# Optimization experiments

Measured on AMD Instinct MI355X. Metric: run time of the kernel, lower is better.

## Reference

```python
import jax, jax.numpy as jnp
import numpy as np

N0, N1, N2 = 120000, 40000, 10000   # sampled node counts per hop
E0, E1 = 600000, 150000             # edges per block (fanout ~15)
DIN, DH, NC = 128, 256, 47


def _glorot(k, fan_in, fan_out):
    s = (2.0 / (fan_in + fan_out)) ** 0.5
    return jax.random.normal(k, (fan_in, fan_out), jnp.float32) * s


def setup_inputs() -> dict:
    key = jax.random.key(0)
    ks = jax.random.split(key, 20)
    x0 = jax.random.normal(ks[0], (N0, DIN), jnp.float32)
    src0 = jax.random.randint(ks[1], (E0,), 0, N0)
    dst0 = jax.random.randint(ks[2], (E0,), 0, N1)
    src1 = jax.random.randint(ks[3], (E1,), 0, N1)
    dst1 = jax.random.randint(ks[4], (E1,), 0, N2)
    srcb0 = jax.random.randint(ks[5], (E0,), 0, N0)
    dstb0 = jax.random.randint(ks[6], (E0,), 0, N1)
    srcb1 = jax.random.randint(ks[7], (E1,), 0, N1)
    dstb1 = jax.random.randint(ks[8], (E1,), 0, N2)
    # id_old_value_new: must satisfy idx[:n] < n for every truncation length n,
    # i.e. idx[k] in [0, k+1)
    rng = np.random.default_rng(0)
    idx = jnp.asarray((rng.random(N0) * (np.arange(N0) + 1)).astype(np.int64))
    mix_ratio = jnp.float32(0.5)
    Wl0 = _glorot(ks[9], DIN, DH); Wr0 = _glorot(ks[10], DIN, DH)
    b0 = jnp.zeros((DH,), jnp.float32)
    Wl1 = _glorot(ks[11], DH, DH); Wr1 = _glorot(ks[12], DH, DH)
    b1 = jnp.zeros((DH,), jnp.float32)
    Wlin = _glorot(ks[13], DH, NC)
    blin = jnp.zeros((NC,), jnp.float32)
    return dict(x0=x0, src0=src0, dst0=dst0, src1=src1, dst1=dst1,
                srcb0=srcb0, dstb0=dstb0, srcb1=srcb1, dstb1=dstb1,
                idx=idx, mix_ratio=mix_ratio,
                Wl0=Wl0, Wr0=Wr0, b0=b0, Wl1=Wl1, Wr1=Wr1, b1=b1,
                Wlin=Wlin, blin=blin)


def _sage(x_all, root_x, src, dst, n_root, Wl, Wr, b):
    # PyG-style SAGEConv, mean aggregation: lin_l(mean_j x_j) + lin_r(root)
    msgs = x_all[src]                                        # [E, D] gather
    s = jax.ops.segment_sum(msgs, dst, num_segments=n_root)  # [n_root, D]
    cnt = jax.ops.segment_sum(jnp.ones_like(dst, dtype=x_all.dtype), dst,
                              num_segments=n_root)
    mean = s / jnp.maximum(cnt, 1.0)[:, None]
    return mean @ Wl + root_x @ Wr + b


def reference(x0, src0, dst0, src1, dst1, srcb0, dstb0, srcb1, dstb1,
              idx, mix_ratio, Wl0, Wr0, b0, Wl1, Wr1, b1, Wlin, blin):
    blocks = [(src0, dst0, N1), (src1, dst1, N2)]
    blocks_b = [(srcb0, dstb0, N1), (srcb1, dstb1, N2)]
    params = [(Wl0, Wr0, b0), (Wl1, Wr1, b1)]
    m = mix_ratio

    # first branch (dropout omitted: inference mode)
    aggr_xs = [x0]
    for i in range(2):
        src, dst, n_root = blocks[i]
        Wl, Wr, b = params[i]
        root_x = aggr_xs[-1][:n_root]
        x = jax.nn.relu(_sage(aggr_xs[-1], root_x, src, dst, n_root, Wl, Wr, b))
        aggr_xs.append(x)

    # permuted branch via id_old_value_new gather
    aggr_xs_b = [x[idx[: x.shape[0]]] for x in aggr_xs]

    x_mix = aggr_xs[0] * m + aggr_xs_b[0] * (1.0 - m)
    for i in range(2):
        src, dst, n_root = blocks[i]
        srcb, dstb, n_root_b = blocks_b[i]
        Wl, Wr, b = params[i]
        x_new = jax.nn.relu(_sage(aggr_xs[i], x_mix[:n_root], src, dst,
                                  n_root, Wl, Wr, b))
        x_new_b = jax.nn.relu(_sage(aggr_xs_b[i], x_mix[:n_root_b], srcb, dstb,
                                    n_root_b, Wl, Wr, b))
        x_mix = x_new * m + x_new_b * (1.0 - m)

    logits = x_mix @ Wlin + blin
    return jax.nn.log_softmax(logits, axis=-1)
```

## Files before the change

### kernel.cpp

```cpp
#include <hip/hip_runtime.h>
#include <math.h>

#define N1C 40000
#define N2C 10000
#define DIN 128
#define DH  256
#define NC  47

#define TOTCNT (2 * N1C + 2 * N2C)
#define CAP 64
#define CURSTR 16

typedef __attribute__((ext_vector_type(8))) short v8s;
typedef __attribute__((ext_vector_type(4))) float v4f;
typedef __attribute__((ext_vector_type(2))) float v2f;

#if __has_builtin(__builtin_amdgcn_cvt_pk_f32_fp8)
#define HW_FP8 1
#endif

__device__ __forceinline__ unsigned short f2bf(float f) {
    unsigned int u = __float_as_uint(f);
    u += 0x7FFF + ((u >> 16) & 1);
    return (unsigned short)(u >> 16);
}
__device__ __forceinline__ float bf2f(unsigned int h) {
    return __uint_as_float(h << 16);
}

__device__ __forceinline__ unsigned char f2e4m3(float f) {
    unsigned int u = __float_as_uint(f);
    unsigned char s = (unsigned char)((u >> 24) & 0x80);
    float a = __uint_as_float(u & 0x7FFFFFFF);
    if (a > 448.0f) a = 448.0f;
    if (a < 0.015625f) {
        int k = (int)rintf(a * 512.0f);
        return s | (unsigned char)k;
    }
    unsigned int bits = __float_as_uint(a);
    int et = (int)(bits >> 23) - 127 + 7;
    unsigned int m32 = bits & 0x7FFFFF;
    unsigned int m3 = m32 >> 20;
    unsigned int rest = m32 & 0xFFFFF;
    if (rest > 0x80000 || (rest == 0x80000 && (m3 & 1))) m3++;
    if (m3 == 8) { m3 = 0; et++; }
    if (et > 15 || (et == 15 && m3 == 7)) return s | 0x7E;
    return s | (unsigned char)((et << 3) | m3);
}

__device__ __forceinline__ void dec4(unsigned int u, float& f0, float& f1,
                                     float& f2, float& f3) {
#ifdef HW_FP8
    v2f lo = __builtin_amdgcn_cvt_pk_f32_fp8((int)u, false);
    v2f hi = __builtin_amdgcn_cvt_pk_f32_fp8((int)u, true);
    f0 = lo[0]; f1 = lo[1]; f2 = hi[0]; f3 = hi[1];
#else
    auto d1 = [](unsigned int b) -> float {
        int e = (b >> 3) & 15, mm = b & 7;
        float d = (e == 0) ? (float)mm * (1.0f / 512.0f)
                           : (1.0f + (float)mm * 0.125f) * exp2f((float)(e - 7));
        return (b & 0x80) ? -d : d;
    };
    f0 = d1(u & 0xFF); f1 = d1((u >> 8) & 0xFF);
    f2 = d1((u >> 16) & 0xFF); f3 = d1(u >> 24);
#endif
}

__global__ __launch_bounds__(256) void front_fused(
        const int* __restrict__ src0, const int* __restrict__ dst0,
        const int* __restrict__ srcb0, const int* __restrict__ dstb0,
        const int* __restrict__ src1, const int* __restrict__ dst1,
        const int* __restrict__ srcb1, const int* __restrict__ dstb1,
        const int* __restrict__ perm, int* __restrict__ cur,
        int* __restrict__ bucket, int E0, int E1, int nbFill,
        const float* __restrict__ x0, unsigned char* __restrict__ x0f,
        long n8, int nbConv,
        const float* __restrict__ Wl0, const float* __restrict__ Wr0,
        const float* __restrict__ Wl1, const float* __restrict__ Wr1,
        unsigned short* __restrict__ Wt0l, unsigned short* __restrict__ Wt0r,
        unsigned short* __restrict__ Wt1l, unsigned short* __restrict__ Wt1r) {
    int b = blockIdx.x, t = threadIdx.x;
    if (b < nbFill) {
        int e = b * 256 + t;
        int tot = 2 * E0 + 2 * E1;
        if (e >= tot) return;
        int s, bin;
        if (e < E0) {
            s = src0[e];                  bin = dst0[e];
        } else if (e < 2 * E0) {
            int le = e - E0;
            s = perm[srcb0[le]];          bin = N1C + dstb0[le];
        } else if (e < 2 * E0 + E1) {
            int le = e - 2 * E0;
            s = src1[le];                 bin = 2 * N1C + dst1[le];
        } else {
            int le = e - 2 * E0 - E1;
            s = perm[srcb1[le]];          bin = 2 * N1C + N2C + dstb1[le];
        }
        int pos = atomicAdd(&cur[(size_t)bin * CURSTR], 1);
        if (pos < CAP) bucket[(size_t)bin * CAP + pos] = s;
    } else if (b < nbFill + nbConv) {
        long i = (long)(b - nbFill) * 256 + t;
        if (i >= n8) return;
        const float4* p = (const float4*)(x0 + i * 8);
        float4 a = p[0], c = p[1];
        float f[8] = {a.x, a.y, a.z, a.w, c.x, c.y, c.z, c.w};
        unsigned int q0 = 0, q1 = 0;
#pragma unroll
        for (int j = 0; j < 8; j++) {
            unsigned int e8 = f2e4m3(f[j]);
            if (j < 4) q0 |= e8 << (8 * j); else q1 |= e8 << (8 * (j - 4));
        }
        uint2 q = {q0, q1};
        *(uint2*)(x0f + i * 8) = q;
    } else {
        int id = (b - nbFill - nbConv) * 256 + t;
        const int S0 = DIN * DH;
        const int S1 = DH * DH;
        const float* W; unsigned short* Wt; int K, loc;
        if (id < S0)                   { W = Wl0; Wt = Wt0l; K = DIN; loc = id; }
        else if (id < 2 * S0)          { W = Wr0; Wt = Wt0r; K = DIN; loc = id - S0; }
        else if (id < 2 * S0 + S1)     { W = Wl1; Wt = Wt1l; K = DH;  loc = id - 2 * S0; }
        else if (id < 2 * S0 + 2 * S1) { W = Wr1; Wt = Wt1r; K = DH;  loc = id - 2 * S0 - S1; }
        else return;
        int n = loc / K, k = loc - n * K;
        Wt[(size_t)n * K + k] = f2bf(W[(size_t)k * DH + n]);
    }
}

__global__ __launch_bounds__(256) void gather_mean_128f(
        const unsigned char* __restrict__ xf, const int* __restrict__ bucket,
        const int* __restrict__ cur, unsigned short* __restrict__ mean0,
        unsigned short* __restrict__ meanb0) {
    const int half = N1C / 8;
    int b = blockIdx.x;
    int binbase; unsigned short* outp; int rb;
    if (b < half) { binbase = 0;   outp = mean0;  rb = b; }
    else          { binbase = N1C; outp = meanb0; rb = b - half; }
    int wv = threadIdx.x >> 6, lane = threadIdx.x & 63;
    int row = rb * 8 + wv * 2 + (lane >> 5);
    int c4 = (lane & 31) * 4;
    int bin = binbase + row;
    int cnt = min(cur[(size_t)bin * CURSTR], CAP);
    const int* cs = bucket + (size_t)bin * CAP;
    float a0 = 0.0f, a1 = 0.0f, a2 = 0.0f, a3 = 0.0f;
    int i = 0;
    for (; i + 3 < cnt; i += 4) {
        int s0 = cs[i], s1 = cs[i + 1], s2 = cs[i + 2], s3 = cs[i + 3];
        unsigned int u = *(const unsigned int*)&xf[(size_t)s0 * DIN + c4];
        unsigned int v = *(const unsigned int*)&xf[(size_t)s1 * DIN + c4];
        unsigned int w = *(const unsigned int*)&xf[(size_t)s2 * DIN + c4];
        unsigned int z = *(const unsigned int*)&xf[(size_t)s3 * DIN + c4];
        float u0, u1, u2, u3, w0, w1, w2, w3, p0, p1, p2, p3, q0, q1, q2, q3;
        dec4(u, u0, u1, u2, u3);
        dec4(v, w0, w1, w2, w3);
        dec4(w, p0, p1, p2, p3);
        dec4(z, q0, q1, q2, q3);
        a0 += (u0 + w0) + (p0 + q0); a1 += (u1 + w1) + (p1 + q1);
        a2 += (u2 + w2) + (p2 + q2); a3 += (u3 + w3) + (p3 + q3);
    }
    for (; i < cnt; i++) {
        unsigned int u = *(const unsigned int*)&xf[(size_t)cs[i] * DIN + c4];
        float u0, u1, u2, u3;
        dec4(u, u0, u1, u2, u3);
        a0 += u0; a1 += u1; a2 += u2; a3 += u3;
    }
    float inv = 1.0f / (float)max(cnt, 1);
    uint2 o;
    o.x = (unsigned int)f2bf(a0 * inv) | ((unsigned int)f2bf(a1 * inv) << 16);
    o.y = (unsigned int)f2bf(a2 * inv) | ((unsigned int)f2bf(a3 * inv) << 16);
    *(uint2*)&outp[(size_t)row * DIN + c4] = o;
}

__global__ __launch_bounds__(256) void gather_mean_256f(
        const unsigned char* __restrict__ xf, const int* __restrict__ bucket,
        const int* __restrict__ cur, unsigned short* __restrict__ mean1,
        unsigned short* __restrict__ meanb1) {
    const int half = N2C / 4;
    int b = blockIdx.x;
    int binbase; unsigned short* outp; int rb;
    if (b < half) { binbase = 2 * N1C;       outp = mean1;  rb = b; }
    else          { binbase = 2 * N1C + N2C; outp = meanb1; rb = b - half; }
    int row = rb * 4 + (threadIdx.x >> 6);
    int lane = threadIdx.x & 63;
    int bin = binbase + row;
    int cnt = min(cur[(size_t)bin * CURSTR], CAP);
    const int* cs = bucket + (size_t)bin * CAP;
    float a0 = 0.0f, a1 = 0.0f, a2 = 0.0f, a3 = 0.0f;
    int i = 0;
    for (; i + 3 < cnt; i += 4) {
        int s0 = cs[i], s1 = cs[i + 1], s2 = cs[i + 2], s3 = cs[i + 3];
        unsigned int u = *(const unsigned int*)&xf[(size_t)s0 * DH + lane * 4];
        unsigned int v = *(const unsigned int*)&xf[(size_t)s1 * DH + lane * 4];
        unsigned int w = *(const unsigned int*)&xf[(size_t)s2 * DH + lane * 4];
        unsigned int z = *(const unsigned int*)&xf[(size_t)s3 * DH + lane * 4];
        float u0, u1, u2, u3, w0, w1, w2, w3, p0, p1, p2, p3, q0, q1, q2, q3;
        dec4(u, u0, u1, u2, u3);
        dec4(v, w0, w1, w2, w3);
        dec4(w, p0, p1, p2, p3);
        dec4(z, q0, q1, q2, q3);
        a0 += (u0 + w0) + (p0 + q0); a1 += (u1 + w1) + (p1 + q1);
        a2 += (u2 + w2) + (p2 + q2); a3 += (u3 + w3) + (p3 + q3);
    }
    for (; i < cnt; i++) {
        unsigned int u = *(const unsigned int*)&xf[(size_t)cs[i] * DH + lane * 4];
        float u0, u1, u2, u3;
        dec4(u, u0, u1, u2, u3);
        a0 += u0; a1 += u1; a2 += u2; a3 += u3;
    }
    float inv = 1.0f / (float)max(cnt, 1);
    uint2 o;
    o.x = (unsigned int)f2bf(a0 * inv) | ((unsigned int)f2bf(a1 * inv) << 16);
    o.y = (unsigned int)f2bf(a2 * inv) | ((unsigned int)f2bf(a3 * inv) << 16);
    *(uint2*)&outp[(size_t)row * DH + lane * 4] = o;
}

#define KP0 136
#define H0T 5
__global__ __launch_bounds__(256, 2) void hop0_mfma(
        const float* __restrict__ x0, const int* __restrict__ idx,
        const unsigned short* __restrict__ mean0, const unsigned short* __restrict__ meanb0,
        const unsigned short* __restrict__ Wtl, const unsigned short* __restrict__ Wtr,
        const float* __restrict__ b, const float* __restrict__ mixp,
        unsigned char* __restrict__ x1f, unsigned short* __restrict__ xm1) {
    __shared__ unsigned short Alds[4][16][KP0];
    int t = threadIdx.x;
    int wv = t >> 6, lane = t & 63;
    int mrow = lane & 15, quad = lane >> 4;
    float m = *mixp;

    v8s wl[4][4], wr[4][4];
    float bb[4];
#pragma unroll
    for (int ct = 0; ct < 4; ct++) {
        int n = wv * 64 + mrow * 4 + ct;
        bb[ct] = b[n];
#pragma unroll
        for (int ks = 0; ks < 4; ks++) {
            int k0 = ks * 32 + quad * 8;
            wl[ct][ks] = *(const v8s*)&Wtl[(size_t)n * DIN + k0];
            wr[ct][ks] = *(const v8s*)&Wtr[(size_t)n * DIN + k0];
        }
    }

    for (int tile = 0; tile < H0T; tile++) {
        int row0 = (blockIdx.x * H0T + tile) * 16;
        {
            int r = t >> 4, k0 = (t & 15) * 8;
            int rg = row0 + r;
            *(v8s*)&Alds[0][r][k0] = *(const v8s*)&mean0[(size_t)rg * DIN + k0];
            *(v8s*)&Alds[1][r][k0] = *(const v8s*)&meanb0[(size_t)rg * DIN + k0];
            const float4* xr4 = (const float4*)&x0[(size_t)rg * DIN + k0];
            float4 A0 = xr4[0], A1 = xr4[1];
            int ib = idx[rg];
            const float4* xb4 = (const float4*)&x0[(size_t)ib * DIN + k0];
            float4 B0 = xb4[0], B1 = xb4[1];
            float fa[8] = {A0.x, A0.y, A0.z, A0.w, A1.x, A1.y, A1.z, A1.w};
            float fb[8] = {B0.x, B0.y, B0.z, B0.w, B1.x, B1.y, B1.z, B1.w};
            v8s vr, vm;
#pragma unroll
            for (int j = 0; j < 8; j++) {
                vr[j] = (short)f2bf(fa[j]);
                vm[j] = (short)f2bf(m * fa[j] + (1.0f - m) * fb[j]);
            }
            *(v8s*)&Alds[2][r][k0] = vr;
            *(v8s*)&Alds[3][r][k0] = vm;
        }
        __syncthreads();
        v4f accA[4], accB[4], accC[4], accD[4];
#pragma unroll
        for (int ct = 0; ct < 4; ct++) {
            accA[ct] = (v4f){0.f, 0.f, 0.f, 0.f}; accB[ct] = (v4f){0.f, 0.f, 0.f, 0.f};
            accC[ct] = (v4f){0.f, 0.f, 0.f, 0.f}; accD[ct] = (v4f){0.f, 0.f, 0.f, 0.f};
        }
#pragma unroll
        for (int ks = 0; ks < 4; ks++) {
            int k0 = ks * 32 + quad * 8;
            v8s aM = *(v8s*)&Alds[0][mrow][k0];
            v8s aB = *(v8s*)&Alds[1][mrow][k0];
            v8s aR = *(v8s*)&Alds[2][mrow][k0];
            v8s aX = *(v8s*)&Alds[3][mrow][k0];
#pragma unroll
            for (int ct = 0; ct < 4; ct++) {
                accA[ct] = __builtin_amdgcn_mfma_f32_16x16x32_bf16(aM, wl[ct][ks], accA[ct], 0, 0, 0);
                accB[ct] = __builtin_amdgcn_mfma_f32_16x16x32_bf16(aB, wl[ct][ks], accB[ct], 0, 0, 0);
                accC[ct] = __builtin_amdgcn_mfma_f32_16x16x32_bf16(aR, wr[ct][ks], accC[ct], 0, 0, 0);
                accD[ct] = __builtin_amdgcn_mfma_f32_16x16x32_bf16(aX, wr[ct][ks], accD[ct], 0, 0, 0);
            }
        }
        int colb = wv * 64 + mrow * 4;
#pragma unroll
        for (int r = 0; r < 4; r++) {
            int row = row0 + quad * 4 + r;
            unsigned int xpack = 0;
            unsigned int s01, s23;
            unsigned short sh[4];
#pragma unroll
            for (int ct = 0; ct < 4; ct++) {
                float pA = accA[ct][r], pB = accB[ct][r], pC = accC[ct][r], pD = accD[ct][r];
                float xv  = fmaxf(pA + pC + bb[ct], 0.0f);
                float xn  = fmaxf(pA + pD + bb[ct], 0.0f);
                float xnb = fmaxf(pB + pD + bb[ct], 0.0f);
                xpack |= ((unsigned int)f2e4m3(xv)) << (8 * ct);
                sh[ct] = f2bf(m * xn + (1.0f - m) * xnb);
            }
            s01 = (unsigned int)sh[0] | ((unsigned int)sh[1] << 16);
            s23 = (unsigned int)sh[2] | ((unsigned int)sh[3] << 16);
            *(unsigned int*)&x1f[(size_t)row * DH + colb] = xpack;
            uint2 xm = {s01, s23};
            *(uint2*)&xm1[(size_t)row * DH + colb] = xm;
        }
        __syncthreads();
    }
}

#define KP1 264
#define H1T 2
__global__ __launch_bounds__(256, 2) void hop1_mfma(
        const unsigned short* __restrict__ mean1, const unsigned short* __restrict__ meanb1,
        const unsigned short* __restrict__ xm1,
        const unsigned short* __restrict__ Wtl, const unsigned short* __restrict__ Wtr,
        const float* __restrict__ b, const float* __restrict__ mixp,
        float* __restrict__ xm2) {
    __shared__ unsigned short Alds[3][16][KP1];
    int t = threadIdx.x;
    int wv = t >> 6, lane = t & 63;
    int mrow = lane & 15, quad = lane >> 4;
    float m = *mixp;

    v8s wlc[4][4], wrc[4][4];
    float bb[4];
#pragma unroll
    for (int ct = 0; ct < 4; ct++) {
        int n = wv * 64 + mrow * 4 + ct;
        bb[ct] = b[n];
#pragma unroll
        for (int ks = 0; ks < 4; ks++) {
            int k0 = ks * 32 + quad * 8;
            wlc[ct][ks] = *(const v8s*)&Wtl[(size_t)n * DH + k0];
            wrc[ct][ks] = *(const v8s*)&Wtr[(size_t)n * DH + k0];
        }
    }

    for (int tt = 0; tt < H1T; tt++) {
        int tIdx = blockIdx.x * H1T + tt;
        if (tIdx >= N2C / 16) break;
        int row0 = tIdx * 16;
        {
            int r = t >> 4, k0 = (t & 15) * 16;
            int rg = row0 + r;
            *(v8s*)&Alds[0][r][k0]     = *(const v8s*)&mean1[(size_t)rg * DH + k0];
            *(v8s*)&Alds[0][r][k0 + 8] = *(const v8s*)&mean1[(size_t)rg * DH + k0 + 8];
            *(v8s*)&Alds[1][r][k0]     = *(const v8s*)&meanb1[(size_t)rg * DH + k0];
            *(v8s*)&Alds[1][r][k0 + 8] = *(const v8s*)&meanb1[(size_t)rg * DH + k0 + 8];
            *(v8s*)&Alds[2][r][k0]     = *(const v8s*)&xm1[(size_t)rg * DH + k0];
            *(v8s*)&Alds[2][r][k0 + 8] = *(const v8s*)&xm1[(size_t)rg * DH + k0 + 8];
        }
        __syncthreads();
        v4f accA[4], accB[4], accC[4];
#pragma unroll
        for (int ct = 0; ct < 4; ct++) {
            accA[ct] = (v4f){0.f, 0.f, 0.f, 0.f};
            accB[ct] = (v4f){0.f, 0.f, 0.f, 0.f};
            accC[ct] = (v4f){0.f, 0.f, 0.f, 0.f};
        }
#pragma unroll
        for (int ks = 0; ks < 8; ks++) {
            int k0 = ks * 32 + quad * 8;
            v8s aM = *(v8s*)&Alds[0][mrow][k0];
            v8s aB = *(v8s*)&Alds[1][mrow][k0];
            v8s aR = *(v8s*)&Alds[2][mrow][k0];
#pragma unroll
            for (int ct = 0; ct < 4; ct++) {
                v8s bl, br;
                if (ks < 4) { bl = wlc[ct][ks]; br = wrc[ct][ks]; }
                else {
                    int n = wv * 64 + mrow * 4 + ct;
                    bl = *(const v8s*)&Wtl[(size_t)n * DH + k0];
                    br = *(const v8s*)&Wtr[(size_t)n * DH + k0];
                }
                accA[ct] = __builtin_amdgcn_mfma_f32_16x16x32_bf16(aM, bl, accA[ct], 0, 0, 0);
                accB[ct] = __builtin_amdgcn_mfma_f32_16x16x32_bf16(aB, bl, accB[ct], 0, 0, 0);
                accC[ct] = __builtin_amdgcn_mfma_f32_16x16x32_bf16(aR, br, accC[ct], 0, 0, 0);
            }
        }
        int colb = wv * 64 + mrow * 4;
#pragma unroll
        for (int r = 0; r < 4; r++) {
            int row = row0 + quad * 4 + r;
            float4 o;
            float v0 = fmaxf(accA[0][r] + accC[0][r] + bb[0], 0.0f);
            float w0 = fmaxf(accB[0][r] + accC[0][r] + bb[0], 0.0f);
            float v1 = fmaxf(accA[1][r] + accC[1][r] + bb[1], 0.0f);
            float w1 = fmaxf(accB[1][r] + accC[1][r] + bb[1], 0.0f);
            float v2 = fmaxf(accA[2][r] + accC[2][r] + bb[2], 0.0f);
            float w2 = fmaxf(accB[2][r] + accC[2][r] + bb[2], 0.0f);
            float v3 = fmaxf(accA[3][r] + accC[3][r] + bb[3], 0.0f);
            float w3 = fmaxf(accB[3][r] + accC[3][r] + bb[3], 0.0f);
            o.x = m * v0 + (1.0f - m) * w0;
            o.y = m * v1 + (1.0f - m) * w1;
            o.z = m * v2 + (1.0f - m) * w2;
            o.w = m * v3 + (1.0f - m) * w3;
            *(float4*)&xm2[(size_t)row * DH + colb] = o;
        }
        __syncthreads();
    }
}

__global__ __launch_bounds__(256) void logits_lsm(
        const float* __restrict__ xmix2, const float* __restrict__ Wlin,
        const float* __restrict__ blin, float* __restrict__ out, int nrows) {
    int w = threadIdx.x >> 6;
    int row = blockIdx.x * 4 + w;
    int t = threadIdx.x & 63;
    __shared__ float xs[4][DH];
    if (row < nrows)
        for (int i = t; i < DH; i += 64) xs[w][i] = xmix2[(size_t)row * DH + i];
    __syncthreads();
    if (row >= nrows) return;
    float acc = 0.0f;
    if (t < NC) {
        acc = blin[t];
        for (int k = 0; k < DH; k++) acc += xs[w][k] * Wlin[k * NC + t];
    }
    float v = (t < NC) ? acc : -INFINITY;
    float mx = v;
    for (int off = 32; off; off >>= 1) mx = fmaxf(mx, __shfl_xor(mx, off, 64));
    float ex = (t < NC) ? expf(acc - mx) : 0.0f;
    float sum = ex;
    for (int off = 32; off; off >>= 1) sum += __shfl_xor(sum, off, 64);
    if (t < NC) out[(size_t)row * NC + t] = acc - mx - logf(sum);
}

extern "C" void kernel_launch(void* const* d_in, const int* in_sizes, int n_in,
                              void* d_out, int out_size, void* d_ws, size_t ws_size,
                              hipStream_t stream) {
    const float* x0    = (const float*)d_in[0];
    const int*   src0  = (const int*)d_in[1];
    const int*   dst0  = (const int*)d_in[2];
    const int*   src1  = (const int*)d_in[3];
    const int*   dst1  = (const int*)d_in[4];
    const int*   srcb0 = (const int*)d_in[5];
    const int*   dstb0 = (const int*)d_in[6];
    const int*   srcb1 = (const int*)d_in[7];
    const int*   dstb1 = (const int*)d_in[8];
    const int*   idx   = (const int*)d_in[9];
    const float* mixp  = (const float*)d_in[10];
    const float* Wl0   = (const float*)d_in[11];
    const float* Wr0   = (const float*)d_in[12];
    const float* b0    = (const float*)d_in[13];
    const float* Wl1   = (const float*)d_in[14];
    const float* Wr1   = (const float*)d_in[15];
    const float* b1    = (const float*)d_in[16];
    const float* Wlin  = (const float*)d_in[17];
    const float* blin  = (const float*)d_in[18];
    float* out = (float*)d_out;

    const int E0 = in_sizes[1];
    const int E1 = in_sizes[3];
    const long x0elems = (long)in_sizes[0];

    int* wsi    = (int*)d_ws;
    int* cur    = wsi;
    int* bucket = cur + (size_t)TOTCNT * CURSTR;
    unsigned short* wsh = (unsigned short*)(bucket + (size_t)TOTCNT * CAP);
    unsigned short* mean0  = wsh;
    unsigned short* meanb0 = mean0  + (size_t)N1C * DIN;
    unsigned short* mean1  = meanb0 + (size_t)N1C * DIN;
    unsigned short* meanb1 = mean1  + (size_t)N2C * DH;
    unsigned short* xm1h   = meanb1 + (size_t)N2C * DH;
    unsigned short* Wt0l   = xm1h   + (size_t)N1C * DH;
    unsigned short* Wt0r   = Wt0l + DIN * DH;
    unsigned short* Wt1l   = Wt0r + DIN * DH;
    unsigned short* Wt1r   = Wt1l + DH * DH;
    float* xm2 = (float*)(Wt1r + DH * DH);
    unsigned char* x0f = (unsigned char*)(xm2 + (size_t)N2C * DH);
    unsigned char* x1f = x0f + (size_t)x0elems;

    hipMemsetAsync(cur, 0, sizeof(int) * (size_t)TOTCNT * CURSTR, stream);

    int etot = 2 * E0 + 2 * E1;
    int nbFill = (etot + 255) / 256;
    long n8 = x0elems / 8;
    int nbConv = (int)((n8 + 255) / 256);
    int nbW = (2 * DIN * DH + 2 * DH * DH + 255) / 256;
    front_fused<<<nbFill + nbConv + nbW, 256, 0, stream>>>(
        src0, dst0, srcb0, dstb0, src1, dst1, srcb1, dstb1, idx, cur, bucket,
        E0, E1, nbFill, x0, x0f, n8, nbConv,
        Wl0, Wr0, Wl1, Wr1, Wt0l, Wt0r, Wt1l, Wt1r);

    gather_mean_128f<<<2 * (N1C / 8), 256, 0, stream>>>(x0f, bucket, cur, mean0, meanb0);

    hop0_mfma<<<N1C / (16 * H0T), 256, 0, stream>>>(x0, idx, mean0, meanb0, Wt0l, Wt0r,
                                                    b0, mixp, x1f, xm1h);

    gather_mean_256f<<<2 * (N2C / 4), 256, 0, stream>>>(x1f, bucket, cur, mean1, meanb1);

    hop1_mfma<<<(N2C / 16 + H1T - 1) / H1T, 256, 0, stream>>>(mean1, meanb1, xm1h,
                                                              Wt1l, Wt1r, b1, mixp, xm2);

    logits_lsm<<<(N2C + 3) / 4, 256, 0, stream>>>(xm2, Wlin, blin, out, N2C);
}
```

Before: 341.5 us.

## Move hop-1 bucket fill and weight conversion into hop-0 gather kernel

New measurement: 348.3 us. About the same (+2.0%).

```diff
diff --git a/kernel.cpp b/kernel.cpp
--- a/kernel.cpp
+++ b/kernel.cpp
@@ -69,52 +69,81 @@
 __global__ __launch_bounds__(256) void front_fused(
         const int* __restrict__ src0, const int* __restrict__ dst0,
         const int* __restrict__ srcb0, const int* __restrict__ dstb0,
+        const int* __restrict__ perm, int* __restrict__ cur,
+        int* __restrict__ bucket, int E0, int nbFillA,
+        const float* __restrict__ x0, unsigned char* __restrict__ x0f,
+        long n8) {
+    int b = blockIdx.x, t = threadIdx.x;
+    if (b < nbFillA) {
+        int tot = 2 * E0;
+        int base = b * 512;
+#pragma unroll
+        for (int j = 0; j < 2; j++) {
+            int e = base + j * 256 + t;
+            if (e < tot) {
+                int s, bin;
+                if (e < E0) {
+                    s = src0[e];                  bin = dst0[e];
+                } else {
+                    int le = e - E0;
+                    s = perm[srcb0[le]];          bin = N1C + dstb0[le];
+                }
+                int pos = atomicAdd(&cur[(size_t)bin * CURSTR], 1);
+                if (pos < CAP) bucket[(size_t)bin * CAP + pos] = s;
+            }
+        }
+    } else {
+        long i = (long)(b - nbFillA) * 256 + t;
+        if (i >= n8) return;
+        const float4* p = (const float4*)(x0 + i * 8);
+        float4 a = p[0], c = p[1];
+        float f[8] = {a.x, a.y, a.z, a.w, c.x, c.y, c.z, c.w};
+        unsigned int q0 = 0, q1 = 0;
+#pragma unroll
+        for (int j = 0; j < 8; j++) {
+            unsigned int e8 = f2e4m3(f[j]);
+            if (j < 4) q0 |= e8 << (8 * j); else q1 |= e8 << (8 * (j - 4));
+        }
+        uint2 q = {q0, q1};
+        *(uint2*)(x0f + i * 8) = q;
+    }
+}
+
+__global__ __launch_bounds__(256) void gather_front(
+        const unsigned char* __restrict__ xf, const int* __restrict__ bucket,
+        int* __restrict__ cur, unsigned short* __restrict__ mean0,
+        unsigned short* __restrict__ meanb0,
         const int* __restrict__ src1, const int* __restrict__ dst1,
         const int* __restrict__ srcb1, const int* __restrict__ dstb1,
-        const int* __restrict__ perm, int* __restrict__ cur,
-        int* __restrict__ bucket, int E0, int E1, int nbFill,
-        const float* __restrict__ x0, unsigned char* __restrict__ x0f,
-        long n8, int nbConv,
+        const int* __restrict__ perm, int* __restrict__ bucketw,
+        int E1, int nbFillB, int nbW,
         const float* __restrict__ Wl0, const float* __restrict__ Wr0,
         const float* __restrict__ Wl1, const float* __restrict__ Wr1,
         unsigned short* __restrict__ Wt0l, unsigned short* __restrict__ Wt0r,
         unsigned short* __restrict__ Wt1l, unsigned short* __restrict__ Wt1r) {
     int b = blockIdx.x, t = threadIdx.x;
-    if (b < nbFill) {
-        int e = b * 256 + t;
-        int tot = 2 * E0 + 2 * E1;
-        if (e >= tot) return;
-        int s, bin;
-        if (e < E0) {
-            s = src0[e];                  bin = dst0[e];
-        } else if (e < 2 * E0) {
-            int le = e - E0;
-            s = perm[srcb0[le]];          bin = N1C + dstb0[le];
-        } else if (e < 2 * E0 + E1) {
-            int le = e - 2 * E0;
-            s = src1[le];                 bin = 2 * N1C + dst1[le];
-        } else {
-            int le = e - 2 * E0 - E1;
-            s = perm[srcb1[le]];          bin = 2 * N1C + N2C + dstb1[le];
-        }
-        int pos = atomicAdd(&cur[(size_t)bin * CURSTR], 1);
-        if (pos < CAP) bucket[(size_t)bin * CAP + pos] = s;
-    } else if (b < nbFill + nbConv) {
-        long i = (long)(b - nbFill) * 256 + t;
-        if (i >= n8) return;
-        const float4* p = (const float4*)(x0 + i * 8);
-        float4 a = p[0], c = p[1];
-        float f[8] = {a.x, a.y, a.z, a.w, c.x, c.y, c.z, c.w};
-        unsigned int q0 = 0, q1 = 0;
-#pragma unroll
-        for (int j = 0; j < 8; j++) {
-            unsigned int e8 = f2e4m3(f[j]);
-            if (j < 4) q0 |= e8 << (8 * j); else q1 |= e8 << (8 * (j - 4));
-        }
-        uint2 q = {q0, q1};
-        *(uint2*)(x0f + i * 8) = q;
-    } else {
-        int id = (b - nbFill - nbConv) * 256 + t;
+    if (b < nbFillB) {
+        int tot = 2 * E1;
+        int base = b * 512;
+#pragma unroll
+        for (int j = 0; j < 2; j++) {
+            int e = base + j * 256 + t;
+            if (e < tot) {
+                int s, bin;
+                if (e < E1) {
+                    s = src1[e];                  bin = 2 * N1C + dst1[e];
+                } else {
+                    int le = e - E1;
+                    s = perm[srcb1[le]];          bin = 2 * N1C + N2C + dstb1[le];
+                }
+                int pos = atomicAdd(&cur[(size_t)bin * CURSTR], 1);
+                if (pos < CAP) bucketw[(size_t)bin * CAP + pos] = s;
+            }
+        }
+        return;
+    }
+    if (b < nbFillB + nbW) {
+        int id = (b - nbFillB) * 256 + t;
         const int S0 = DIN * DH;
         const int S1 = DH * DH;
         const float* W; unsigned short* Wt; int K, loc;
@@ -125,19 +154,14 @@
         else return;
         int n = loc / K, k = loc - n * K;
         Wt[(size_t)n * K + k] = f2bf(W[(size_t)k * DH + n]);
-    }
-}
-
-__global__ __launch_bounds__(256) void gather_mean_128f(
-        const unsigned char* __restrict__ xf, const int* __restrict__ bucket,
-        const int* __restrict__ cur, unsigned short* __restrict__ mean0,
-        unsigned short* __restrict__ meanb0) {
+        return;
+    }
+    int gb = b - nbFillB - nbW;
     const int half = N1C / 8;
-    int b = blockIdx.x;
     int binbase; unsigned short* outp; int rb;
-    if (b < half) { binbase = 0;   outp = mean0;  rb = b; }
-    else          { binbase = N1C; outp = meanb0; rb = b - half; }
-    int wv = threadIdx.x >> 6, lane = threadIdx.x & 63;
+    if (gb < half) { binbase = 0;   outp = mean0;  rb = gb; }
+    else           { binbase = N1C; outp = meanb0; rb = gb - half; }
+    int wv = t >> 6, lane = t & 63;
     int row = rb * 8 + wv * 2 + (lane >> 5);
     int c4 = (lane & 31) * 4;
     int bin = binbase + row;
@@ -479,17 +503,18 @@
 
     hipMemsetAsync(cur, 0, sizeof(int) * (size_t)TOTCNT * CURSTR, stream);
 
-    int etot = 2 * E0 + 2 * E1;
-    int nbFill = (etot + 255) / 256;
+    int nbFillA = (2 * E0 + 511) / 512;
     long n8 = x0elems / 8;
     int nbConv = (int)((n8 + 255) / 256);
+    front_fused<<<nbFillA + nbConv, 256, 0, stream>>>(
+        src0, dst0, srcb0, dstb0, idx, cur, bucket, E0, nbFillA, x0, x0f, n8);
+
+    int nbFillB = (2 * E1 + 511) / 512;
     int nbW = (2 * DIN * DH + 2 * DH * DH + 255) / 256;
-    front_fused<<<nbFill + nbConv + nbW, 256, 0, stream>>>(
-        src0, dst0, srcb0, dstb0, src1, dst1, srcb1, dstb1, idx, cur, bucket,
-        E0, E1, nbFill, x0, x0f, n8, nbConv,
+    gather_front<<<nbFillB + nbW + 2 * (N1C / 8), 256, 0, stream>>>(
+        x0f, bucket, cur, mean0, meanb0,
+        src1, dst1, srcb1, dstb1, idx, bucket, E1, nbFillB, nbW,
         Wl0, Wr0, Wl1, Wr1, Wt0l, Wt0r, Wt1l, Wt1r);
-
-    gather_mean_128f<<<2 * (N1C / 8), 256, 0, stream>>>(x0f, bucket, cur, mean0, meanb0);
 
     hop0_mfma<<<N1C / (16 * H0T), 256, 0, stream>>>(x0, idx, mean0, meanb0, Wt0l, Wt0r,
                                                     b0, mixp, x1f, xm1h);
```
